# Kernel tuning notes

Hardware: AMD Instinct MI355X
Metric: run time of the kernel (lower is better)

Reference implementation:

```python
import jax, jax.numpy as jnp
import numpy as np

EMBED_DIM = 1024
HEADS = 16
HD = EMBED_DIM // HEADS

def setup_inputs() -> dict:
    key = jax.random.key(0)
    ks = jax.random.split(key, 6)
    s = 1.0 / np.sqrt(EMBED_DIM)
    x = jax.random.normal(ks[0], (4, 2048, EMBED_DIM), dtype=jnp.float32)
    Wq = jax.random.uniform(ks[1], (EMBED_DIM, EMBED_DIM), jnp.float32, -s, s)
    Wk = jax.random.uniform(ks[2], (EMBED_DIM, EMBED_DIM), jnp.float32, -s, s)
    Wv = jax.random.uniform(ks[3], (EMBED_DIM, EMBED_DIM), jnp.float32, -s, s)
    Wo = jax.random.uniform(ks[4], (EMBED_DIM, EMBED_DIM), jnp.float32, -s, s)
    bo = jax.random.uniform(ks[5], (EMBED_DIM,), jnp.float32, -s, s)
    return {"x": x, "Wq": Wq, "Wk": Wk, "Wv": Wv, "Wo": Wo, "bo": bo}

def reference(x, Wq, Wk, Wv, Wo, bo):
    B, S, E = x.shape
    # projections (torch Linear: y = x @ W.T), split into heads -> [B,H,S,hd]
    def proj(W):
        return (x @ W.T).reshape(B, S, HEADS, HD).transpose(0, 2, 1, 3)
    q, k, v = proj(Wq), proj(Wk), proj(Wv)
    energy = jnp.einsum('bhid,bhjd->bhij', q, k) / np.sqrt(HD).astype(np.float32)
    causal = jnp.tril(jnp.ones((S, S), dtype=bool))
    energy = jnp.where(causal, energy, -jnp.inf)
    attn = jax.nn.softmax(energy, axis=-1)  # dropout omitted (eval mode)
    out = jnp.einsum('bhij,bhjd->bhid', attn, v)
    out = out.transpose(0, 2, 1, 3).reshape(B, S, E)
    return out @ Wo.T + bo
```

## Files before the change

### kernel.cpp

```cpp
#include <hip/hip_runtime.h>
#include <math.h>

#define EMB   1024
#define HEADS 16
#define HD    64
#define SEQ   2048
#define BATCH 4
#define MTOT  (BATCH * SEQ)
#define XSZ   ((size_t)MTOT * EMB)
#define WSZ   ((size_t)EMB * EMB)

typedef __attribute__((ext_vector_type(8))) short s16x8;
typedef __attribute__((ext_vector_type(4))) short s16x4;
typedef __attribute__((ext_vector_type(4))) float f32x4;

__device__ __forceinline__ short f2bf(float f) {
    unsigned u = __builtin_bit_cast(unsigned, f);
    u += 0x7fffu + ((u >> 16) & 1u);
    return (short)(u >> 16);
}

__device__ __forceinline__ unsigned pk_bf16(float a, float b) {
#if __has_builtin(__builtin_amdgcn_cvt_pk_bf16_f32)
    typedef __attribute__((ext_vector_type(2))) __bf16 bf16x2;
    return __builtin_bit_cast(unsigned, __builtin_amdgcn_cvt_pk_bf16_f32(a, b));
#else
    return (unsigned)(unsigned short)f2bf(a) |
           ((unsigned)(unsigned short)f2bf(b) << 16);
#endif
}

__device__ __forceinline__ float fexp2(float x) {
#if __has_builtin(__builtin_amdgcn_exp2f)
    return __builtin_amdgcn_exp2f(x);
#else
    return exp2f(x);
#endif
}

__device__ __forceinline__ void async16(const void* g, void* l) {
    __builtin_amdgcn_global_load_lds(
        (const __attribute__((address_space(1))) unsigned*)g,
        (__attribute__((address_space(3))) unsigned*)l, 16, 0, 0);
}

__global__ __launch_bounds__(256)
void cvt_inputs(const float* __restrict__ x,  const float* __restrict__ wq,
                const float* __restrict__ wk, const float* __restrict__ wv,
                const float* __restrict__ wo, short* __restrict__ xb,
                short* __restrict__ wcat)
{
    const size_t e = ((size_t)blockIdx.x * 256 + threadIdx.x) * 8;
    const float* src;
    short* dst;
    float scale = 1.0f;
    if (e < XSZ) {
        src = x + e;
        dst = xb + e;
    } else {
        const size_t r = e - XSZ;
        const int w = (int)(r >> 20);
        const size_t off = r & (WSZ - 1);
        src = (w == 0 ? wq : w == 1 ? wk : w == 2 ? wv : wo) + off;
        dst = wcat + r;
        if (w == 0) scale = 0.125f * 1.44269504f;
    }
    const float4 a = ((const float4*)src)[0];
    const float4 b = ((const float4*)src)[1];
    s16x8 v;
    v[0] = f2bf(a.x * scale); v[1] = f2bf(a.y * scale);
    v[2] = f2bf(a.z * scale); v[3] = f2bf(a.w * scale);
    v[4] = f2bf(b.x * scale); v[5] = f2bf(b.y * scale);
    v[6] = f2bf(b.z * scale); v[7] = f2bf(b.w * scale);
    *(s16x8*)dst = v;
}

template<bool OUT_BF16>
__global__ __launch_bounds__(256)
void gemm_bf16(const short* __restrict__ A, const short* __restrict__ B,
               void* __restrict__ C, int ldc, const float* __restrict__ bias,
               int K)
{
    __shared__ short lA[128 * 32];
    __shared__ short lB[128 * 32];

    const int tid  = threadIdx.x;
    const int wv   = tid >> 6;
    const int lane = tid & 63;
    const int col  = lane & 15;
    const int quad = lane >> 4;

    const int rowBase = blockIdx.y * 128;
    const int colBase = blockIdx.x * 128;

    const int srow = tid >> 2;
    const int skO  = (tid & 3) * 8;

    const short* gA = A + (size_t)(rowBase + srow) * K + skO;
    const short* gB = B + (size_t)(colBase + srow) * K + skO;

    const int m0 = (wv >> 1) * 64;
    const int n0 = (wv & 1) * 64;

    f32x4 acc[4][4];
#pragma unroll
    for (int i = 0; i < 4; ++i)
#pragma unroll
        for (int j = 0; j < 4; ++j) acc[i][j] = (f32x4){0.f, 0.f, 0.f, 0.f};

    for (int k0 = 0; k0 < K; k0 += 32) {
        async16(gA + k0,                 (char*)lA + wv * 1024);
        async16(gA + k0 + (size_t)64 * K, (char*)lA + 4096 + wv * 1024);
        async16(gB + k0,                 (char*)lB + wv * 1024);
        async16(gB + k0 + (size_t)64 * K, (char*)lB + 4096 + wv * 1024);
        __syncthreads();

        s16x8 af[4], bf[4];
#pragma unroll
        for (int i = 0; i < 4; ++i)
            af[i] = *(const s16x8*)&lA[(m0 + i * 16 + col) * 32 + quad * 8];
#pragma unroll
        for (int j = 0; j < 4; ++j)
            bf[j] = *(const s16x8*)&lB[(n0 + j * 16 + col) * 32 + quad * 8];
#pragma unroll
        for (int i = 0; i < 4; ++i)
#pragma unroll
            for (int j = 0; j < 4; ++j)
                acc[i][j] = __builtin_amdgcn_mfma_f32_16x16x32_bf16(af[i], bf[j], acc[i][j], 0, 0, 0);
        __syncthreads();
    }

    if (OUT_BF16) {
        short* Cb = (short*)C;
#pragma unroll
        for (int i = 0; i < 4; ++i) {
            const int rg = rowBase + m0 + i * 16 + quad * 4;
#pragma unroll
            for (int j = 0; j < 4; ++j) {
                const int cg = colBase + n0 + j * 16 + col;
#pragma unroll
                for (int r = 0; r < 4; ++r)
                    Cb[(size_t)(rg + r) * ldc + cg] = f2bf(acc[i][j][r]);
            }
        }
    } else {
        float* Cf = (float*)C;
#pragma unroll
        for (int j = 0; j < 4; ++j) {
            const int cg = colBase + n0 + j * 16 + col;
            const float bj = bias ? bias[cg] : 0.f;
#pragma unroll
            for (int i = 0; i < 4; ++i) {
                const int rg = rowBase + m0 + i * 16 + quad * 4;
#pragma unroll
                for (int r = 0; r < 4; ++r)
                    Cf[(size_t)(rg + r) * ldc + cg] = acc[i][j][r] + bj;
            }
        }
    }
}

#define LDQ 3072
__global__ __launch_bounds__(512)
void attn_mfma(const short* __restrict__ QKV, short* __restrict__ O)
{
    __shared__ short lK[64 * 72];
    __shared__ short lV[64 * 72];
    __shared__ short lP[8 * 32 * 72];

    const int tid  = threadIdx.x;
    const int wv   = tid >> 6;
    const int lane = tid & 63;
    const int col  = lane & 15;
    const int quad = lane >> 4;

    const int bh = blockIdx.y;
    const int b  = bh >> 4;
    const int h  = bh & 15;
    const size_t baseq = (size_t)b * SEQ * LDQ + (size_t)h * HD;
    const size_t basek = baseq + 1024;
    const size_t basev = baseq + 2048;
    const size_t baseo = (size_t)b * SEQ * EMB + (size_t)h * HD;

    const int krow = tid >> 3;
    const int kc0  = (tid & 7) * 8;
    short* pwave = &lP[(wv * 32) * 72];

    const s16x8 onesv = {0x3F80, 0x3F80, 0x3F80, 0x3F80,
                         0x3F80, 0x3F80, 0x3F80, 0x3F80};

    for (int half = 0; half < 2; ++half) {
        const int qsuper = half ? (7 - (int)blockIdx.x) : (int)blockIdx.x;
        const int qb = qsuper * 256;
        const int qlo_w = qb + wv * 32;

        s16x8 qf[2][2];
#pragma unroll
        for (int rb = 0; rb < 2; ++rb) {
            const short* qr = QKV + baseq + (size_t)(qlo_w + rb * 16 + col) * LDQ;
            qf[rb][0] = *(const s16x8*)(qr + quad * 8);
            qf[rb][1] = *(const s16x8*)(qr + 32 + quad * 8);
        }

        f32x4 of[2][4], lsum[2];
#pragma unroll
        for (int rb = 0; rb < 2; ++rb) {
#pragma unroll
            for (int u = 0; u < 4; ++u) of[rb][u] = (f32x4){0.f, 0.f, 0.f, 0.f};
            lsum[rb] = (f32x4){0.f, 0.f, 0.f, 0.f};
        }

        const int nt = qb / 64 + 4;

        s16x8 pk = *(const s16x8*)(QKV + basek + (size_t)krow * LDQ + kc0);
        s16x8 pv = *(const s16x8*)(QKV + basev + (size_t)lane * LDQ + wv * 8);

        for (int kt = 0; kt < nt; ++kt) {
            const int kb = kt * 64;
            __syncthreads();
            *(s16x8*)&lK[krow * 72 + kc0] = pk;
#pragma unroll
            for (int t = 0; t < 8; ++t)
                lV[(wv * 8 + t) * 72 + lane] = pv[t];
            __syncthreads();

            if (kt + 1 < nt) {
                pk = *(const s16x8*)(QKV + basek + (size_t)(kb + 64 + krow) * LDQ + kc0);
                pv = *(const s16x8*)(QKV + basev + (size_t)(kb + 64 + lane) * LDQ + wv * 8);
            }

            if (kb > qlo_w + 31) continue;

            s16x8 kf[4][2];
#pragma unroll
            for (int t = 0; t < 4; ++t) {
                kf[t][0] = *(const s16x8*)&lK[(t * 16 + col) * 72 + quad * 8];
                kf[t][1] = *(const s16x8*)&lK[(t * 16 + col) * 72 + 32 + quad * 8];
            }

#pragma unroll
            for (int rb = 0; rb < 2; ++rb) {
                const int qlo = qlo_w + rb * 16;
                const int qg  = qlo + col;

                f32x4 s[4];
#pragma unroll
                for (int t = 0; t < 4; ++t) {
                    f32x4 acc = (f32x4){0.f, 0.f, 0.f, 0.f};
                    acc = __builtin_amdgcn_mfma_f32_16x16x32_bf16(kf[t][0], qf[rb][0], acc, 0, 0, 0);
                    acc = __builtin_amdgcn_mfma_f32_16x16x32_bf16(kf[t][1], qf[rb][1], acc, 0, 0, 0);
                    s[t] = acc;
                }

                if (kb + 63 > qlo) {
#pragma unroll
                    for (int t = 0; t < 4; ++t)
#pragma unroll
                        for (int rr = 0; rr < 4; ++rr) {
                            const int kg = kb + t * 16 + quad * 4 + rr;
                            if (kg > qg) s[t][rr] = -3.0e38f;
                        }
                }

                short* pbase = pwave + (rb * 16) * 72;
#pragma unroll
                for (int t = 0; t < 4; ++t) {
                    uint2 pkd;
                    pkd.x = pk_bf16(fexp2(s[t][0]), fexp2(s[t][1]));
                    pkd.y = pk_bf16(fexp2(s[t][2]), fexp2(s[t][3]));
                    *(uint2*)&pbase[col * 72 + t * 16 + quad * 4] = pkd;
                }
            }

#pragma unroll
            for (int c = 0; c < 2; ++c) {
                s16x8 vf[4];
#pragma unroll
                for (int u = 0; u < 4; ++u)
                    vf[u] = *(const s16x8*)&lV[(u * 16 + col) * 72 + c * 32 + quad * 8];
#pragma unroll
                for (int rb = 0; rb < 2; ++rb) {
                    const s16x8 pa = *(const s16x8*)&pwave[(rb * 16 + col) * 72 + c * 32 + quad * 8];
                    lsum[rb] = __builtin_amdgcn_mfma_f32_16x16x32_bf16(onesv, pa, lsum[rb], 0, 0, 0);
#pragma unroll
                    for (int u = 0; u < 4; ++u)
                        of[rb][u] = __builtin_amdgcn_mfma_f32_16x16x32_bf16(vf[u], pa, of[rb][u], 0, 0, 0);
                }
            }
        }

#pragma unroll
        for (int rb = 0; rb < 2; ++rb) {
            const float rl = 1.f / lsum[rb][0];
            short* orow = O + baseo + (size_t)(qlo_w + rb * 16 + col) * EMB + quad * 4;
#pragma unroll
            for (int u = 0; u < 4; ++u) {
                uint2 pkd;
                pkd.x = pk_bf16(of[rb][u][0] * rl, of[rb][u][1] * rl);
                pkd.y = pk_bf16(of[rb][u][2] * rl, of[rb][u][3] * rl);
                *(uint2*)&orow[u * 16] = pkd;
            }
        }
    }
}

extern "C" void kernel_launch(void* const* d_in, const int* in_sizes, int n_in,
                              void* d_out, int out_size, void* d_ws, size_t ws_size,
                              hipStream_t stream)
{
    const float* x  = (const float*)d_in[0];
    const float* Wq = (const float*)d_in[1];
    const float* Wk = (const float*)d_in[2];
    const float* Wv = (const float*)d_in[3];
    const float* Wo = (const float*)d_in[4];
    const float* bo = (const float*)d_in[5];
    float* out = (float*)d_out;

    short* xb   = (short*)d_ws;
    short* wcat = xb + XSZ;
    short* qkv  = wcat + 4 * WSZ;
    short* ob   = qkv + (size_t)MTOT * 3 * EMB;

    const int cvt_blocks = (int)((XSZ + 4 * WSZ) / 8 / 256);
    cvt_inputs<<<cvt_blocks, 256, 0, stream>>>(x, Wq, Wk, Wv, Wo, xb, wcat);

    gemm_bf16<true><<<dim3(3072 / 128, MTOT / 128), 256, 0, stream>>>(
        xb, wcat, qkv, 3072, nullptr, EMB);

    attn_mfma<<<dim3(4, BATCH * HEADS), 512, 0, stream>>>(qkv, ob);

    gemm_bf16<false><<<dim3(EMB / 128, MTOT / 128), 256, 0, stream>>>(
        ob, wcat + (size_t)3 * WSZ, out, EMB, bo, EMB);
}
```

Baseline: 265.5 us.

## Replace bf16 GEMM with 256x256 double-buffered 8-phase pipelined kernel

Replaces the simple 128x128 single-stage GEMM used for the QKV and output projections with a 256x256-tile, 512-thread kernel. It double-buffers LDS across K=64 halves, interleaves async global loads with MFMA quarters under explicit barriers and waitcnts, and uses XOR-swizzled LDS addressing plus a workgroup remap for L2 locality. The aim is to hide global-load latency, raise arithmetic intensity per LDS byte, and remove the sync-per-32-K stall of the old loop. In exchange it uses 128KB LDS and many accumulator registers, and the hand-placed wait counts and barriers are fragile. The output projection also drops to only 128 workgroups.

```diff
diff --git a/kernel.cpp b/kernel.cpp
--- a/kernel.cpp
+++ b/kernel.cpp
@@ -75,86 +75,169 @@
     *(s16x8*)dst = v;
 }
 
+#define BAR() __builtin_amdgcn_s_barrier()
+#define WAIT_LGKM() do { asm volatile("s_waitcnt lgkmcnt(0)" ::: "memory"); \
+                         __builtin_amdgcn_sched_barrier(0); } while (0)
+#define WAIT_VM(n) asm volatile("s_waitcnt vmcnt(" #n ")" ::: "memory")
+
+#define RD_A(ldsX, qm) \
+    _Pragma("unroll") for (int mi = 0; mi < 4; ++mi) \
+    _Pragma("unroll") for (int kk = 0; kk < 2; ++kk) \
+        a[mi][kk] = *(const s16x8*)((ldsX) + ((qm)*8 + wm*4 + mi) * 2048 + kk * 1024 + abase);
+
+#define RD_B(ldsX, qn, breg) \
+    _Pragma("unroll") for (int ni = 0; ni < 2; ++ni) \
+    _Pragma("unroll") for (int kk = 0; kk < 2; ++kk) \
+        breg[ni][kk] = *(const s16x8*)((ldsX) + ((qn)*8 + wn*2 + ni) * 2048 + kk * 1024 + abase);
+
+#define MFMA_Q(qm, qn, breg) \
+    __builtin_amdgcn_s_setprio(1); \
+    _Pragma("unroll") for (int mi = 0; mi < 4; ++mi) \
+    _Pragma("unroll") for (int ni = 0; ni < 2; ++ni) \
+    _Pragma("unroll") for (int kk = 0; kk < 2; ++kk) \
+        acc[(qm)*4+mi][(qn)*2+ni] = __builtin_amdgcn_mfma_f32_16x16x32_bf16( \
+            a[mi][kk], breg[ni][kk], acc[(qm)*4+mi][(qn)*2+ni], 0, 0, 0); \
+    __builtin_amdgcn_s_setprio(0);
+
+#define STAGE(pM, ldsMat, h, k0) do { \
+    async16((pM) + (size_t)((h) * 128) * K + (k0),      (ldsMat) + (h) * 16384 + wv1024); \
+    async16((pM) + (size_t)((h) * 128 + 64) * K + (k0), (ldsMat) + (h) * 16384 + 8192 + wv1024); \
+} while (0)
+
 template<bool OUT_BF16>
-__global__ __launch_bounds__(256)
-void gemm_bf16(const short* __restrict__ A, const short* __restrict__ B,
-               void* __restrict__ C, int ldc, const float* __restrict__ bias,
-               int K)
+__global__ __launch_bounds__(512, 2)
+void gemm_8ph(const short* __restrict__ A, const short* __restrict__ B,
+              void* __restrict__ C, int ldc, const float* __restrict__ bias,
+              int K)
 {
-    __shared__ short lA[128 * 32];
-    __shared__ short lB[128 * 32];
-
-    const int tid  = threadIdx.x;
-    const int wv   = tid >> 6;
-    const int lane = tid & 63;
-    const int col  = lane & 15;
-    const int quad = lane >> 4;
-
-    const int rowBase = blockIdx.y * 128;
-    const int colBase = blockIdx.x * 128;
-
-    const int srow = tid >> 2;
-    const int skO  = (tid & 3) * 8;
-
-    const short* gA = A + (size_t)(rowBase + srow) * K + skO;
-    const short* gB = B + (size_t)(colBase + srow) * K + skO;
-
-    const int m0 = (wv >> 1) * 64;
-    const int n0 = (wv & 1) * 64;
-
-    f32x4 acc[4][4];
-#pragma unroll
-    for (int i = 0; i < 4; ++i)
+    __shared__ __align__(16) char lds[131072];
+    char* ldsA0 = lds;
+    char* ldsB0 = lds + 32768;
+    char* ldsA1 = lds + 65536;
+    char* ldsB1 = lds + 98304;
+
+    const int tid   = threadIdx.x;
+    const int wv    = tid >> 6;
+    const int lane  = tid & 63;
+    const int col16 = lane & 15;
+    const int quad  = lane >> 4;
+    const int wm    = wv >> 2;
+    const int wn    = wv & 3;
+    const int wv1024 = wv << 10;
+
+    const int nwg = gridDim.x * gridDim.y;
+    int wg = blockIdx.y * gridDim.x + blockIdx.x;
+    wg = (wg & 7) * (nwg >> 3) + (wg >> 3);
+    const int rowBase = (wg / gridDim.x) * 256;
+    const int colBase = (wg % gridDim.x) * 256;
+
+    const int abase = (col16 * 64 + quad * 16) ^ ((col16 & 8) << 2);
+
+    const int rlane = (lane >> 2) & 15;
+    const int rw0   = ((wv >> 1) << 4) + rlane;
+    const int colSt = ((wv & 1) << 5) + (((lane & 3) << 3) ^ ((lane & 32) >> 1));
+    const short* pA = A + (size_t)(rowBase + rw0) * K + colSt;
+    const short* pB = B + (size_t)(colBase + rw0) * K + colSt;
+
+    s16x8 a[4][2], bq0[2][2], bq1[2][2];
+    f32x4 acc[8][4];
+#pragma unroll
+    for (int i = 0; i < 8; ++i)
 #pragma unroll
         for (int j = 0; j < 4; ++j) acc[i][j] = (f32x4){0.f, 0.f, 0.f, 0.f};
 
-    for (int k0 = 0; k0 < K; k0 += 32) {
-        async16(gA + k0,                 (char*)lA + wv * 1024);
-        async16(gA + k0 + (size_t)64 * K, (char*)lA + 4096 + wv * 1024);
-        async16(gB + k0,                 (char*)lB + wv * 1024);
-        async16(gB + k0 + (size_t)64 * K, (char*)lB + 4096 + wv * 1024);
-        __syncthreads();
-
-        s16x8 af[4], bf[4];
-#pragma unroll
-        for (int i = 0; i < 4; ++i)
-            af[i] = *(const s16x8*)&lA[(m0 + i * 16 + col) * 32 + quad * 8];
-#pragma unroll
-        for (int j = 0; j < 4; ++j)
-            bf[j] = *(const s16x8*)&lB[(n0 + j * 16 + col) * 32 + quad * 8];
-#pragma unroll
-        for (int i = 0; i < 4; ++i)
-#pragma unroll
-            for (int j = 0; j < 4; ++j)
-                acc[i][j] = __builtin_amdgcn_mfma_f32_16x16x32_bf16(af[i], bf[j], acc[i][j], 0, 0, 0);
-        __syncthreads();
+    const int NITER = K >> 7;
+
+    STAGE(pA, ldsA0, 0, 0);
+    STAGE(pA, ldsA0, 1, 0);
+    STAGE(pB, ldsB0, 0, 0);
+    STAGE(pB, ldsB0, 1, 0);
+    STAGE(pA, ldsA1, 0, 64);
+    STAGE(pB, ldsB1, 0, 64);
+    WAIT_VM(4);
+    BAR();
+
+    for (int it = 0; it < NITER; ++it) {
+        const int k0 = it << 7;
+        const bool more = (it + 1 < NITER);
+
+        RD_A(ldsA0, 0); RD_B(ldsB0, 0, bq0);
+        STAGE(pA, ldsA1, 1, k0 + 64);
+        BAR(); WAIT_LGKM();
+        MFMA_Q(0, 0, bq0);
+        BAR();
+        RD_B(ldsB0, 1, bq1);
+        STAGE(pB, ldsB1, 1, k0 + 64);
+        BAR(); WAIT_LGKM();
+        MFMA_Q(0, 1, bq1);
+        BAR();
+        RD_A(ldsA0, 1);
+        if (more) STAGE(pA, ldsA0, 0, k0 + 128);
+        BAR(); WAIT_LGKM();
+        MFMA_Q(1, 0, bq0);
+        BAR();
+        if (more) STAGE(pB, ldsB0, 0, k0 + 128);
+        BAR();
+        MFMA_Q(1, 1, bq1);
+        if (more) { WAIT_VM(4); } else { WAIT_VM(0); }
+        BAR();
+        RD_A(ldsA1, 0); RD_B(ldsB1, 0, bq0);
+        if (more) STAGE(pA, ldsA0, 1, k0 + 128);
+        BAR(); WAIT_LGKM();
+        MFMA_Q(0, 0, bq0);
+        BAR();
+        RD_B(ldsB1, 1, bq1);
+        if (more) STAGE(pB, ldsB0, 1, k0 + 128);
+        BAR(); WAIT_LGKM();
+        MFMA_Q(0, 1, bq1);
+        BAR();
+        RD_A(ldsA1, 1);
+        if (more) STAGE(pA, ldsA1, 0, k0 + 192);
+        BAR(); WAIT_LGKM();
+        MFMA_Q(1, 0, bq0);
+        BAR();
+        if (more) STAGE(pB, ldsB1, 0, k0 + 192);
+        BAR();
+        MFMA_Q(1, 1, bq1);
+        WAIT_VM(4);
+        BAR();
     }
 
     if (OUT_BF16) {
         short* Cb = (short*)C;
 #pragma unroll
-        for (int i = 0; i < 4; ++i) {
-            const int rg = rowBase + m0 + i * 16 + quad * 4;
-#pragma unroll
-            for (int j = 0; j < 4; ++j) {
-                const int cg = colBase + n0 + j * 16 + col;
+        for (int qm = 0; qm < 2; ++qm)
+#pragma unroll
+        for (int mi = 0; mi < 4; ++mi) {
+            const int rg0 = rowBase + qm * 128 + wm * 64 + mi * 16 + quad * 4;
+#pragma unroll
+            for (int qn = 0; qn < 2; ++qn)
+#pragma unroll
+            for (int ni = 0; ni < 2; ++ni) {
+                const int cg = colBase + qn * 128 + wn * 32 + ni * 16 + col16;
+                const f32x4 v = acc[qm * 4 + mi][qn * 2 + ni];
 #pragma unroll
                 for (int r = 0; r < 4; ++r)
-                    Cb[(size_t)(rg + r) * ldc + cg] = f2bf(acc[i][j][r]);
+                    Cb[(size_t)(rg0 + r) * ldc + cg] = f2bf(v[r]);
             }
         }
     } else {
         float* Cf = (float*)C;
 #pragma unroll
-        for (int j = 0; j < 4; ++j) {
-            const int cg = colBase + n0 + j * 16 + col;
+        for (int qn = 0; qn < 2; ++qn)
+#pragma unroll
+        for (int ni = 0; ni < 2; ++ni) {
+            const int cg = colBase + qn * 128 + wn * 32 + ni * 16 + col16;
             const float bj = bias ? bias[cg] : 0.f;
 #pragma unroll
-            for (int i = 0; i < 4; ++i) {
-                const int rg = rowBase + m0 + i * 16 + quad * 4;
+            for (int qm = 0; qm < 2; ++qm)
+#pragma unroll
+            for (int mi = 0; mi < 4; ++mi) {
+                const int rg0 = rowBase + qm * 128 + wm * 64 + mi * 16 + quad * 4;
+                const f32x4 v = acc[qm * 4 + mi][qn * 2 + ni];
 #pragma unroll
                 for (int r = 0; r < 4; ++r)
-                    Cf[(size_t)(rg + r) * ldc + cg] = acc[i][j][r] + bj;
+                    Cf[(size_t)(rg0 + r) * ldc + cg] = v[r] + bj;
             }
         }
     }
@@ -324,11 +407,11 @@
     const int cvt_blocks = (int)((XSZ + 4 * WSZ) / 8 / 256);
     cvt_inputs<<<cvt_blocks, 256, 0, stream>>>(x, Wq, Wk, Wv, Wo, xb, wcat);
 
-    gemm_bf16<true><<<dim3(3072 / 128, MTOT / 128), 256, 0, stream>>>(
+    gemm_8ph<true><<<dim3(3072 / 256, MTOT / 256), 512, 0, stream>>>(
         xb, wcat, qkv, 3072, nullptr, EMB);
 
     attn_mfma<<<dim3(4, BATCH * HEADS), 512, 0, stream>>>(qkv, ob);
 
-    gemm_bf16<false><<<dim3(EMB / 128, MTOT / 128), 256, 0, stream>>>(
+    gemm_8ph<false><<<dim3(EMB / 256, MTOT / 256), 512, 0, stream>>>(
         ob, wcat + (size_t)3 * WSZ, out, EMB, bo, EMB);
 }
```

Result: faster. 251.7 us (-5.2%).
